# Kernel optimization log

Measured on AMD Instinct MI355X. Metric: run time of the kernel, lower is better.

The kernel has to match this reference:

```python
import jax, jax.numpy as jnp
import numpy as np

B, N, DIN, H, A = 4096, 32, 256, 128, 32  # batch, n_agents, din, hidden_dim, n_actions
NEG = 9e15


def _linear_params(key, fan_in, fan_out):
    kw, kb = jax.random.split(key)
    bound = 1.0 / np.sqrt(fan_in)
    w = jax.random.uniform(kw, (fan_in, fan_out), jnp.float32, -bound, bound)
    b = jax.random.uniform(kb, (fan_out,), jnp.float32, -bound, bound)
    return w, b


def setup_inputs() -> dict:
    key = jax.random.key(0)
    ks = jax.random.split(key, 12)
    x = jax.random.normal(ks[0], (B, N, DIN), jnp.float32)
    mask = jax.random.randint(ks[1], (B, N, N), 0, 2).astype(jnp.float32)
    enc_w, enc_b = _linear_params(ks[2], DIN, H)
    a1_vw, a1_vb = _linear_params(ks[3], H, H)
    a1_kw, a1_kb = _linear_params(ks[4], H, H)
    a1_qw, a1_qb = _linear_params(ks[5], H, H)
    a1_ow, a1_ob = _linear_params(ks[6], H, H)
    a2_vw, a2_vb = _linear_params(ks[7], H, H)
    a2_kw, a2_kb = _linear_params(ks[8], H, H)
    a2_qw, a2_qb = _linear_params(ks[9], H, H)
    a2_ow, a2_ob = _linear_params(ks[10], H, H)
    q_w, q_b = _linear_params(ks[11], H, A)
    return dict(x=x, mask=mask, enc_w=enc_w, enc_b=enc_b,
                a1_vw=a1_vw, a1_vb=a1_vb, a1_kw=a1_kw, a1_kb=a1_kb,
                a1_qw=a1_qw, a1_qb=a1_qb, a1_ow=a1_ow, a1_ob=a1_ob,
                a2_vw=a2_vw, a2_vb=a2_vb, a2_kw=a2_kw, a2_kb=a2_kb,
                a2_qw=a2_qw, a2_qb=a2_qb, a2_ow=a2_ow, a2_ob=a2_ob,
                q_w=q_w, q_b=q_b)


def _att_block(h, mask, vw, vb, kw, kb, qw, qb, ow, ob):
    # h: [B, N, H]; mask: [B, N, N]
    v = jax.nn.relu(jnp.einsum('bnd,dh->bnh', h, vw) + vb)
    q = jax.nn.relu(jnp.einsum('bnd,dh->bnh', h, qw) + qb)
    k = jax.nn.relu(jnp.einsum('bnd,dh->bnh', h, kw) + kb)
    scores = jnp.einsum('bih,bjh->bij', q, k)               # [B, N, N]
    logits = scores * mask - NEG * (1.0 - mask)
    att = jax.nn.softmax(logits, axis=2)
    out = jnp.einsum('bij,bjh->bih', att, v)
    return jax.nn.relu(jnp.einsum('bnh,ho->bno', out, ow) + ob)


def reference(x, mask, enc_w, enc_b,
              a1_vw, a1_vb, a1_kw, a1_kb, a1_qw, a1_qb, a1_ow, a1_ob,
              a2_vw, a2_vb, a2_kw, a2_kb, a2_qw, a2_qb, a2_ow, a2_ob,
              q_w, q_b):
    h1 = jax.nn.relu(jnp.einsum('bnd,dh->bnh', x, enc_w) + enc_b)
    h2 = _att_block(h1, mask, a1_vw, a1_vb, a1_kw, a1_kb, a1_qw, a1_qb, a1_ow, a1_ob)
    h3 = _att_block(h2, mask, a2_vw, a2_vb, a2_kw, a2_kb, a2_qw, a2_qb, a2_ow, a2_ob)
    q = jnp.einsum('bnh,ha->bna', h3, q_w) + q_b            # [B, N, A]
    return q
```

## Files before the change

kernel.cpp:

```cpp
#include <hip/hip_runtime.h>
#include <hip/hip_bf16.h>

typedef __attribute__((ext_vector_type(8))) short bf16x8;
typedef __attribute__((ext_vector_type(4))) short bf16x4;
typedef __attribute__((ext_vector_type(4))) float f32x4;

#define DEVI static __device__ __forceinline__

constexpr int NAG = 32, DIN = 256, HDIM = 128, ADIM = 32;
constexpr int G = 2;

constexpr int WS_ENC = 0;
constexpr int WS_H   = 32768;
constexpr int WS_QW  = 32768 + 8 * 16384;
constexpr int WS_TOT = WS_QW + 4096;

constexpr int SH = 136;
constexpr int SV = 72;
constexpr int SA = 40;
constexpr int SX = 264;

constexpr int L_R0 = 0;
constexpr int L_R1 = 17408;
constexpr int L_R2 = 34816;
constexpr int L_RV = 52224;
constexpr int L_AT = 70656;
constexpr int L_TOT = 75776;

DEVI short f2bf(float f) {
  union { float f; unsigned u; } a; a.f = f;
  return (short)((a.u + 0x7fffu + ((a.u >> 16) & 1u)) >> 16);
}

__global__ void prep_weights(const float* __restrict__ enc_w,
                             const float* __restrict__ m0, const float* __restrict__ m1,
                             const float* __restrict__ m2, const float* __restrict__ m3,
                             const float* __restrict__ m4, const float* __restrict__ m5,
                             const float* __restrict__ m6, const float* __restrict__ m7,
                             const float* __restrict__ qw,
                             short* __restrict__ ws)
{
  const int blk = blockIdx.x, tid = threadIdx.x;
  const float* src; int base, NM, nsh, f4;
  if (blk < 32) { src = enc_w; base = WS_ENC; NM = 8; nsh = 7; f4 = blk * 256 + tid; }
  else if (blk < 160) {
    const int m = (blk - 32) >> 4;
    if      (m == 0) src = m0; else if (m == 1) src = m1;
    else if (m == 2) src = m2; else if (m == 3) src = m3;
    else if (m == 4) src = m4; else if (m == 5) src = m5;
    else if (m == 6) src = m6; else             src = m7;
    base = WS_H + (m << 14); NM = 8; nsh = 7; f4 = ((blk - 32) & 15) * 256 + tid;
  } else { src = qw; base = WS_QW; NM = 2; nsh = 5; f4 = (blk - 160) * 256 + tid; }
  const int s = f4 * 4;
  const int row = s >> nsh, col0 = s & ((1 << nsh) - 1);
  const float4 v = *(const float4*)(src + s);
  const int j = row & 7, ks = row >> 5, lhi = ((row >> 3) & 3) * 16;
  const float vv[4] = {v.x, v.y, v.z, v.w};
#pragma unroll
  for (int c = 0; c < 4; ++c) {
    const int col = col0 + c;
    const int mt = col >> 4, lane = lhi + (col & 15);
    ws[base + (((ks * NM + mt) * 64 + lane) << 3) + j] = f2bf(vv[c]);
  }
}

template<int KSTEPS, bool RELU>
DEVI void linearSw(const short* __restrict__ src, int sstride,
                   const short* __restrict__ wfrag, const float* __restrict__ bias,
                   short* __restrict__ dst,
                   int wave, int lr, int lq, int lane)
{
  const int mg = wave >> 1, ng = wave & 1;
  f32x4 acc[2][2];
#pragma unroll
  for (int a = 0; a < 2; ++a)
#pragma unroll
    for (int b = 0; b < 2; ++b) acc[a][b] = (f32x4){0.f, 0.f, 0.f, 0.f};

  const bf16x8* wp = (const bf16x8*)wfrag;
#pragma unroll
  for (int ks = 0; ks < KSTEPS; ++ks) {
    bf16x8 hb[2];
#pragma unroll
    for (int b = 0; b < 2; ++b)
      hb[b] = *(const bf16x8*)(src + ((ng * 2 + b) * 16 + lr) * sstride + ks * 32 + lq * 8);
    bf16x8 wa[2];
#pragma unroll
    for (int a = 0; a < 2; ++a)
      wa[a] = wp[(ks * 8 + mg * 2 + a) * 64 + lane];
#pragma unroll
    for (int a = 0; a < 2; ++a)
#pragma unroll
      for (int b = 0; b < 2; ++b)
        acc[a][b] = __builtin_amdgcn_mfma_f32_16x16x32_bf16(wa[a], hb[b], acc[a][b], 0, 0, 0);
  }
#pragma unroll
  for (int a = 0; a < 2; ++a) {
    const float4 bv = *(const float4*)(bias + (mg * 2 + a) * 16 + lq * 4);
    const float bb[4] = {bv.x, bv.y, bv.z, bv.w};
#pragma unroll
    for (int b = 0; b < 2; ++b) {
      bf16x4 s;
#pragma unroll
      for (int r = 0; r < 4; ++r) {
        float v = acc[a][b][r] + bb[r];
        if (RELU) v = fmaxf(v, 0.f);
        s[r] = f2bf(v);
      }
      *(bf16x4*)(dst + ((ng * 2 + b) * 16 + lr) * SH + (mg * 2 + a) * 16 + lq * 4) = s;
    }
  }
}

DEVI void qkv_pass(const short* __restrict__ h,
                   const short* __restrict__ wq, const short* __restrict__ wk,
                   const short* __restrict__ wv,
                   const float* __restrict__ bq, const float* __restrict__ bk,
                   const float* __restrict__ bv,
                   short* __restrict__ Q, short* __restrict__ K, short* __restrict__ V,
                   int wave, int lr, int lq, int lane)
{
  const int mg = wave >> 1, ng = wave & 1;
  f32x4 qa[2][2], ka[2][2], va[2][2];
#pragma unroll
  for (int a = 0; a < 2; ++a)
#pragma unroll
    for (int b = 0; b < 2; ++b) {
      qa[a][b] = (f32x4){0.f, 0.f, 0.f, 0.f};
      ka[a][b] = (f32x4){0.f, 0.f, 0.f, 0.f};
      va[a][b] = (f32x4){0.f, 0.f, 0.f, 0.f};
    }
  const bf16x8* wpq = (const bf16x8*)wq;
  const bf16x8* wpk = (const bf16x8*)wk;
  const bf16x8* wpv = (const bf16x8*)wv;
#pragma unroll
  for (int ks = 0; ks < 4; ++ks) {
    bf16x8 hf[2];
#pragma unroll
    for (int b = 0; b < 2; ++b)
      hf[b] = *(const bf16x8*)(h + ((ng * 2 + b) * 16 + lr) * SH + ks * 32 + lq * 8);
#pragma unroll
    for (int a = 0; a < 2; ++a) {
      const bf16x8 wqf = wpq[(ks * 8 + mg * 2 + a) * 64 + lane];
      const bf16x8 wkf = wpk[(ks * 8 + mg * 2 + a) * 64 + lane];
      const bf16x8 wvf = wpv[(ks * 8 + mg * 2 + a) * 64 + lane];
#pragma unroll
      for (int b = 0; b < 2; ++b) {
        qa[a][b] = __builtin_amdgcn_mfma_f32_16x16x32_bf16(wqf, hf[b], qa[a][b], 0, 0, 0);
        ka[a][b] = __builtin_amdgcn_mfma_f32_16x16x32_bf16(wkf, hf[b], ka[a][b], 0, 0, 0);
        va[b][a] = __builtin_amdgcn_mfma_f32_16x16x32_bf16(hf[b], wvf, va[b][a], 0, 0, 0);
      }
    }
  }
#pragma unroll
  for (int a = 0; a < 2; ++a) {
    const float4 bq4 = *(const float4*)(bq + (mg * 2 + a) * 16 + lq * 4);
    const float4 bk4 = *(const float4*)(bk + (mg * 2 + a) * 16 + lq * 4);
    const float qb4[4] = {bq4.x, bq4.y, bq4.z, bq4.w};
    const float kb4[4] = {bk4.x, bk4.y, bk4.z, bk4.w};
#pragma unroll
    for (int b = 0; b < 2; ++b) {
      bf16x4 sq, sk;
#pragma unroll
      for (int r = 0; r < 4; ++r) {
        sq[r] = f2bf(fmaxf(qa[a][b][r] + qb4[r], 0.f));
        sk[r] = f2bf(fmaxf(ka[a][b][r] + kb4[r], 0.f));
      }
      const int off = ((ng * 2 + b) * 16 + lr) * SH + (mg * 2 + a) * 16 + lq * 4;
      *(bf16x4*)(Q + off) = sq;
      *(bf16x4*)(K + off) = sk;
    }
  }
#pragma unroll
  for (int a = 0; a < 2; ++a) {
    const float bvv = bv[(mg * 2 + a) * 16 + lr];
#pragma unroll
    for (int b = 0; b < 2; ++b) {
      bf16x4 sv;
#pragma unroll
      for (int r = 0; r < 4; ++r)
        sv[r] = f2bf(fmaxf(va[b][a][r] + bvv, 0.f));
      *(bf16x4*)(V + ((mg * 2 + a) * 16 + lr) * SV + (ng * 2 + b) * 16 + lq * 4) = sv;
    }
  }
}

DEVI void scores_pass(const short* __restrict__ Q, const short* __restrict__ K,
                      short* __restrict__ AT, const float* __restrict__ mask, int b0,
                      int wave, int lr, int lq, int lane)
{
  const int g = wave >> 1, qt = wave & 1;
  f32x4 sc[2];
  sc[0] = (f32x4){0.f, 0.f, 0.f, 0.f};
  sc[1] = (f32x4){0.f, 0.f, 0.f, 0.f};
#pragma unroll
  for (int ks = 0; ks < 4; ++ks) {
    const bf16x8 qf = *(const bf16x8*)(Q + (g * 32 + qt * 16 + lr) * SH + ks * 32 + lq * 8);
#pragma unroll
    for (int kt = 0; kt < 2; ++kt) {
      const bf16x8 kf = *(const bf16x8*)(K + (g * 32 + kt * 16 + lr) * SH + ks * 32 + lq * 8);
      sc[kt] = __builtin_amdgcn_mfma_f32_16x16x32_bf16(kf, qf, sc[kt], 0, 0, 0);
    }
  }
  const float* mp = mask + (size_t)(b0 + g) * (NAG * NAG) + (qt * 16 + lr) * 32;
  float l[2][4];
  float M = -3.0e38f;
#pragma unroll
  for (int kt = 0; kt < 2; ++kt) {
    const float4 m4 = *(const float4*)(mp + kt * 16 + lq * 4);
    const float mm[4] = {m4.x, m4.y, m4.z, m4.w};
#pragma unroll
    for (int r = 0; r < 4; ++r) {
      const float v = sc[kt][r] * mm[r] - 9e15f * (1.f - mm[r]);
      l[kt][r] = v;
      M = fmaxf(M, v);
    }
  }
  M = fmaxf(M, __shfl_xor(M, 16));
  M = fmaxf(M, __shfl_xor(M, 32));
  float e[2][4], T = 0.f;
#pragma unroll
  for (int kt = 0; kt < 2; ++kt)
#pragma unroll
    for (int r = 0; r < 4; ++r) { e[kt][r] = __expf(l[kt][r] - M); T += e[kt][r]; }
  T += __shfl_xor(T, 16);
  T += __shfl_xor(T, 32);
  const float rT = __frcp_rn(T);
#pragma unroll
  for (int kt = 0; kt < 2; ++kt) {
    bf16x4 s;
#pragma unroll
    for (int r = 0; r < 4; ++r) s[r] = f2bf(e[kt][r] * rT);
    *(bf16x4*)(AT + (g * 32 + qt * 16 + lr) * SA + kt * 16 + lq * 4) = s;
  }
}

DEVI void pv_pass(const short* __restrict__ V, const short* __restrict__ AT,
                  short* __restrict__ AO, int wave, int lr, int lq, int lane)
{
  const int g = wave >> 2, qt = (wave >> 1) & 1, fh = wave & 1;
  const bf16x8 atf = *(const bf16x8*)(AT + (g * 32 + qt * 16 + lr) * SA + lq * 8);
  f32x4 pacc[4];
#pragma unroll
  for (int f = 0; f < 4; ++f) {
    const int ft = fh * 4 + f;
    const bf16x8 vf = *(const bf16x8*)(V + (ft * 16 + lr) * SV + g * 32 + lq * 8);
    pacc[f] = __builtin_amdgcn_mfma_f32_16x16x32_bf16(
        vf, atf, (f32x4){0.f, 0.f, 0.f, 0.f}, 0, 0, 0);
  }
#pragma unroll
  for (int f = 0; f < 4; ++f) {
    const int ft = fh * 4 + f;
    bf16x4 s;
#pragma unroll
    for (int r = 0; r < 4; ++r) s[r] = f2bf(pacc[f][r]);
    *(bf16x4*)(AO + (g * 32 + qt * 16 + lr) * SH + ft * 16 + lq * 4) = s;
  }
}

DEVI void att_block(short* Rh, short* Rq, short* RK, short* RV_, short* ATb,
                    const short* wv, const short* wk, const short* wq, const short* wo,
                    const float* bv, const float* bk, const float* bq, const float* bo,
                    const float* __restrict__ mask, int b0,
                    int wave, int lr, int lq, int lane)
{
  qkv_pass(Rh, wq, wk, wv, bq, bk, bv, Rq, RK, RV_, wave, lr, lq, lane);
  __syncthreads();
  if (wave < 4) scores_pass(Rq, RK, ATb, mask, b0, wave, lr, lq, lane);
  __syncthreads();
  pv_pass(RV_, ATb, Rh, wave, lr, lq, lane);
  __syncthreads();
  linearSw<4, true>(Rh, SH, wo, bo, Rq, wave, lr, lq, lane);
  __syncthreads();
}

__global__ __launch_bounds__(512, 4)
void dgn_main(const float* __restrict__ x, const float* __restrict__ mask,
              const float* __restrict__ enc_b,
              const float* __restrict__ b1v, const float* __restrict__ b1k,
              const float* __restrict__ b1q, const float* __restrict__ b1o,
              const float* __restrict__ b2v, const float* __restrict__ b2k,
              const float* __restrict__ b2q, const float* __restrict__ b2o,
              const float* __restrict__ qb,
              const short* __restrict__ wf,
              float* __restrict__ out)
{
  __shared__ __align__(16) char smem[L_TOT];
  short* R0 = (short*)(smem + L_R0);
  short* R1 = (short*)(smem + L_R1);
  short* R2 = (short*)(smem + L_R2);
  short* RV_ = (short*)(smem + L_RV);
  short* ATb = (short*)(smem + L_AT);
  short* XB = (short*)(smem + L_R1);

  const int tid = threadIdx.x;
  const int wave = tid >> 6, lane = tid & 63;
  const int lr = lane & 15, lq = lane >> 4;
  const int b0 = blockIdx.x * G;

  {
    const float4* xsrc = (const float4*)(x + (size_t)b0 * NAG * DIN);
#pragma unroll
    for (int it = 0; it < 8; ++it) {
      const int q4 = tid + it * 512;
      const float4 v = xsrc[q4];
      bf16x4 s;
      s[0] = f2bf(v.x); s[1] = f2bf(v.y); s[2] = f2bf(v.z); s[3] = f2bf(v.w);
      *(bf16x4*)(XB + (q4 >> 6) * SX + (q4 & 63) * 4) = s;
    }
  }
  __syncthreads();

  linearSw<8, true>(XB, SX, wf + WS_ENC, enc_b, R0, wave, lr, lq, lane);
  __syncthreads();

  att_block(R0, R1, R2, RV_, ATb,
            wf + WS_H + 0 * 16384, wf + WS_H + 1 * 16384,
            wf + WS_H + 2 * 16384, wf + WS_H + 3 * 16384,
            b1v, b1k, b1q, b1o, mask, b0, wave, lr, lq, lane);

  att_block(R1, R0, R2, RV_, ATb,
            wf + WS_H + 4 * 16384, wf + WS_H + 5 * 16384,
            wf + WS_H + 6 * 16384, wf + WS_H + 7 * 16384,
            b2v, b2k, b2q, b2o, mask, b0, wave, lr, lq, lane);

  if (wave < 4) {
    f32x4 ha[2];
    ha[0] = (f32x4){0.f, 0.f, 0.f, 0.f};
    ha[1] = (f32x4){0.f, 0.f, 0.f, 0.f};
    const bf16x8* wp = (const bf16x8*)(wf + WS_QW);
#pragma unroll
    for (int ks = 0; ks < 4; ++ks) {
      const bf16x8 hf = *(const bf16x8*)(R0 + (wave * 16 + lr) * SH + ks * 32 + lq * 8);
#pragma unroll
      for (int a = 0; a < 2; ++a)
        ha[a] = __builtin_amdgcn_mfma_f32_16x16x32_bf16(wp[(ks * 2 + a) * 64 + lane], hf, ha[a], 0, 0, 0);
    }
    const int row = wave * 16 + lr;
    float* op = out + (((size_t)(b0 + (row >> 5)) * NAG) + (row & 31)) * ADIM;
#pragma unroll
    for (int a = 0; a < 2; ++a) {
      const float4 bv4 = *(const float4*)(qb + a * 16 + lq * 4);
      float4 o;
      o.x = ha[a][0] + bv4.x; o.y = ha[a][1] + bv4.y;
      o.z = ha[a][2] + bv4.z; o.w = ha[a][3] + bv4.w;
      *(float4*)(op + a * 16 + lq * 4) = o;
    }
  }
}

extern "C" void kernel_launch(void* const* d_in, const int* in_sizes, int n_in,
                              void* d_out, int out_size, void* d_ws, size_t ws_size,
                              hipStream_t stream)
{
  const float* x     = (const float*)d_in[0];
  const float* mask  = (const float*)d_in[1];
  const float* enc_w = (const float*)d_in[2];
  const float* enc_b = (const float*)d_in[3];
  const float* a1_vw = (const float*)d_in[4];
  const float* a1_vb = (const float*)d_in[5];
  const float* a1_kw = (const float*)d_in[6];
  const float* a1_kb = (const float*)d_in[7];
  const float* a1_qw = (const float*)d_in[8];
  const float* a1_qb = (const float*)d_in[9];
  const float* a1_ow = (const float*)d_in[10];
  const float* a1_ob = (const float*)d_in[11];
  const float* a2_vw = (const float*)d_in[12];
  const float* a2_vb = (const float*)d_in[13];
  const float* a2_kw = (const float*)d_in[14];
  const float* a2_kb = (const float*)d_in[15];
  const float* a2_qw = (const float*)d_in[16];
  const float* a2_qb = (const float*)d_in[17];
  const float* a2_ow = (const float*)d_in[18];
  const float* a2_ob = (const float*)d_in[19];
  const float* q_w   = (const float*)d_in[20];
  const float* q_b   = (const float*)d_in[21];
  short* ws = (short*)d_ws;

  prep_weights<<<164, 256, 0, stream>>>(
      enc_w, a1_vw, a1_kw, a1_qw, a1_ow, a2_vw, a2_kw, a2_qw, a2_ow, q_w, ws);

  dgn_main<<<4096 / G, 512, 0, stream>>>(
      x, mask, enc_b,
      a1_vb, a1_kb, a1_qb, a1_ob,
      a2_vb, a2_kb, a2_qb, a2_ob,
      q_b, ws, (float*)d_out);
}
```

Baseline: 313.2 us.

## Process one batch element per 256-thread block with compact shared-memory layout

Each block now handles a single batch element with 4 waves instead of two elements with 8 waves. Shared-memory buffers are reorganised and aliased (Q/K/V, attention weights and outputs reuse regions), cutting LDS from about 74KB to about 36KB per block. The aim is more resident blocks per CU for better latency hiding. In exchange there are twice as many blocks, weight fragments are reloaded per block, and the softmax stage runs on only 2 of 4 waves.

```diff
diff --git a/kernel.cpp b/kernel.cpp
--- a/kernel.cpp
+++ b/kernel.cpp
@@ -8,7 +8,6 @@
 #define DEVI static __device__ __forceinline__
 
 constexpr int NAG = 32, DIN = 256, HDIM = 128, ADIM = 32;
-constexpr int G = 2;
 
 constexpr int WS_ENC = 0;
 constexpr int WS_H   = 32768;
@@ -16,16 +15,15 @@
 constexpr int WS_TOT = WS_QW + 4096;
 
 constexpr int SH = 136;
-constexpr int SV = 72;
+constexpr int SV = 40;
 constexpr int SA = 40;
 constexpr int SX = 264;
 
-constexpr int L_R0 = 0;
-constexpr int L_R1 = 17408;
-constexpr int L_R2 = 34816;
-constexpr int L_RV = 52224;
-constexpr int L_AT = 70656;
-constexpr int L_TOT = 75776;
+constexpr int L_P0 = 0;
+constexpr int L_P1 = 8704;
+constexpr int L_P2 = 17408;
+constexpr int L_PV = 26112;
+constexpr int L_TOT = 36352;
 
 DEVI short f2bf(float f) {
   union { float f; unsigned u; } a; a.f = f;
@@ -65,12 +63,11 @@
 }
 
 template<int KSTEPS, bool RELU>
-DEVI void linearSw(const short* __restrict__ src, int sstride,
-                   const short* __restrict__ wfrag, const float* __restrict__ bias,
-                   short* __restrict__ dst,
-                   int wave, int lr, int lq, int lane)
-{
-  const int mg = wave >> 1, ng = wave & 1;
+DEVI void linearSw4(const short* __restrict__ src, int sstride,
+                    const short* __restrict__ wfrag, const float* __restrict__ bias,
+                    short* __restrict__ dst,
+                    int mg, int lr, int lq, int lane)
+{
   f32x4 acc[2][2];
 #pragma unroll
   for (int a = 0; a < 2; ++a)
@@ -83,16 +80,14 @@
     bf16x8 hb[2];
 #pragma unroll
     for (int b = 0; b < 2; ++b)
-      hb[b] = *(const bf16x8*)(src + ((ng * 2 + b) * 16 + lr) * sstride + ks * 32 + lq * 8);
-    bf16x8 wa[2];
-#pragma unroll
-    for (int a = 0; a < 2; ++a)
-      wa[a] = wp[(ks * 8 + mg * 2 + a) * 64 + lane];
-#pragma unroll
-    for (int a = 0; a < 2; ++a)
+      hb[b] = *(const bf16x8*)(src + (b * 16 + lr) * sstride + ks * 32 + lq * 8);
+#pragma unroll
+    for (int a = 0; a < 2; ++a) {
+      const bf16x8 wa = wp[(ks * 8 + mg * 2 + a) * 64 + lane];
 #pragma unroll
       for (int b = 0; b < 2; ++b)
-        acc[a][b] = __builtin_amdgcn_mfma_f32_16x16x32_bf16(wa[a], hb[b], acc[a][b], 0, 0, 0);
+        acc[a][b] = __builtin_amdgcn_mfma_f32_16x16x32_bf16(wa, hb[b], acc[a][b], 0, 0, 0);
+    }
   }
 #pragma unroll
   for (int a = 0; a < 2; ++a) {
@@ -107,20 +102,19 @@
         if (RELU) v = fmaxf(v, 0.f);
         s[r] = f2bf(v);
       }
-      *(bf16x4*)(dst + ((ng * 2 + b) * 16 + lr) * SH + (mg * 2 + a) * 16 + lq * 4) = s;
-    }
-  }
-}
-
-DEVI void qkv_pass(const short* __restrict__ h,
-                   const short* __restrict__ wq, const short* __restrict__ wk,
-                   const short* __restrict__ wv,
-                   const float* __restrict__ bq, const float* __restrict__ bk,
-                   const float* __restrict__ bv,
-                   short* __restrict__ Q, short* __restrict__ K, short* __restrict__ V,
-                   int wave, int lr, int lq, int lane)
-{
-  const int mg = wave >> 1, ng = wave & 1;
+      *(bf16x4*)(dst + (b * 16 + lr) * SH + (mg * 2 + a) * 16 + lq * 4) = s;
+    }
+  }
+}
+
+DEVI void qkv_pass4(const short* __restrict__ h,
+                    const short* __restrict__ wq, const short* __restrict__ wk,
+                    const short* __restrict__ wv,
+                    const float* __restrict__ bq, const float* __restrict__ bk,
+                    const float* __restrict__ bv,
+                    short* __restrict__ Q, short* __restrict__ K, short* __restrict__ V,
+                    int mg, int lr, int lq, int lane)
+{
   f32x4 qa[2][2], ka[2][2], va[2][2];
 #pragma unroll
   for (int a = 0; a < 2; ++a)
@@ -138,7 +132,7 @@
     bf16x8 hf[2];
 #pragma unroll
     for (int b = 0; b < 2; ++b)
-      hf[b] = *(const bf16x8*)(h + ((ng * 2 + b) * 16 + lr) * SH + ks * 32 + lq * 8);
+      hf[b] = *(const bf16x8*)(h + (b * 16 + lr) * SH + ks * 32 + lq * 8);
 #pragma unroll
     for (int a = 0; a < 2; ++a) {
       const bf16x8 wqf = wpq[(ks * 8 + mg * 2 + a) * 64 + lane];
@@ -166,7 +160,7 @@
         sq[r] = f2bf(fmaxf(qa[a][b][r] + qb4[r], 0.f));
         sk[r] = f2bf(fmaxf(ka[a][b][r] + kb4[r], 0.f));
       }
-      const int off = ((ng * 2 + b) * 16 + lr) * SH + (mg * 2 + a) * 16 + lq * 4;
+      const int off = (b * 16 + lr) * SH + (mg * 2 + a) * 16 + lq * 4;
       *(bf16x4*)(Q + off) = sq;
       *(bf16x4*)(K + off) = sk;
     }
@@ -180,29 +174,28 @@
 #pragma unroll
       for (int r = 0; r < 4; ++r)
         sv[r] = f2bf(fmaxf(va[b][a][r] + bvv, 0.f));
-      *(bf16x4*)(V + ((mg * 2 + a) * 16 + lr) * SV + (ng * 2 + b) * 16 + lq * 4) = sv;
-    }
-  }
-}
-
-DEVI void scores_pass(const short* __restrict__ Q, const short* __restrict__ K,
-                      short* __restrict__ AT, const float* __restrict__ mask, int b0,
-                      int wave, int lr, int lq, int lane)
-{
-  const int g = wave >> 1, qt = wave & 1;
+      *(bf16x4*)(V + ((mg * 2 + a) * 16 + lr) * SV + b * 16 + lq * 4) = sv;
+    }
+  }
+}
+
+DEVI void scores_pass4(const short* __restrict__ Q, const short* __restrict__ K,
+                       short* __restrict__ AT, const float* __restrict__ mask,
+                       int b0, int qt, int lr, int lq)
+{
   f32x4 sc[2];
   sc[0] = (f32x4){0.f, 0.f, 0.f, 0.f};
   sc[1] = (f32x4){0.f, 0.f, 0.f, 0.f};
 #pragma unroll
   for (int ks = 0; ks < 4; ++ks) {
-    const bf16x8 qf = *(const bf16x8*)(Q + (g * 32 + qt * 16 + lr) * SH + ks * 32 + lq * 8);
+    const bf16x8 qf = *(const bf16x8*)(Q + (qt * 16 + lr) * SH + ks * 32 + lq * 8);
 #pragma unroll
     for (int kt = 0; kt < 2; ++kt) {
-      const bf16x8 kf = *(const bf16x8*)(K + (g * 32 + kt * 16 + lr) * SH + ks * 32 + lq * 8);
+      const bf16x8 kf = *(const bf16x8*)(K + (kt * 16 + lr) * SH + ks * 32 + lq * 8);
       sc[kt] = __builtin_amdgcn_mfma_f32_16x16x32_bf16(kf, qf, sc[kt], 0, 0, 0);
     }
   }
-  const float* mp = mask + (size_t)(b0 + g) * (NAG * NAG) + (qt * 16 + lr) * 32;
+  const float* mp = mask + (size_t)b0 * (NAG * NAG) + (qt * 16 + lr) * 32;
   float l[2][4];
   float M = -3.0e38f;
 #pragma unroll
@@ -231,50 +224,51 @@
     bf16x4 s;
 #pragma unroll
     for (int r = 0; r < 4; ++r) s[r] = f2bf(e[kt][r] * rT);
-    *(bf16x4*)(AT + (g * 32 + qt * 16 + lr) * SA + kt * 16 + lq * 4) = s;
-  }
-}
-
-DEVI void pv_pass(const short* __restrict__ V, const short* __restrict__ AT,
-                  short* __restrict__ AO, int wave, int lr, int lq, int lane)
-{
-  const int g = wave >> 2, qt = (wave >> 1) & 1, fh = wave & 1;
-  const bf16x8 atf = *(const bf16x8*)(AT + (g * 32 + qt * 16 + lr) * SA + lq * 8);
-  f32x4 pacc[4];
-#pragma unroll
-  for (int f = 0; f < 4; ++f) {
-    const int ft = fh * 4 + f;
-    const bf16x8 vf = *(const bf16x8*)(V + (ft * 16 + lr) * SV + g * 32 + lq * 8);
-    pacc[f] = __builtin_amdgcn_mfma_f32_16x16x32_bf16(
-        vf, atf, (f32x4){0.f, 0.f, 0.f, 0.f}, 0, 0, 0);
-  }
-#pragma unroll
-  for (int f = 0; f < 4; ++f) {
-    const int ft = fh * 4 + f;
-    bf16x4 s;
-#pragma unroll
-    for (int r = 0; r < 4; ++r) s[r] = f2bf(pacc[f][r]);
-    *(bf16x4*)(AO + (g * 32 + qt * 16 + lr) * SH + ft * 16 + lq * 4) = s;
-  }
-}
-
-DEVI void att_block(short* Rh, short* Rq, short* RK, short* RV_, short* ATb,
-                    const short* wv, const short* wk, const short* wq, const short* wo,
-                    const float* bv, const float* bk, const float* bq, const float* bo,
-                    const float* __restrict__ mask, int b0,
-                    int wave, int lr, int lq, int lane)
-{
-  qkv_pass(Rh, wq, wk, wv, bq, bk, bv, Rq, RK, RV_, wave, lr, lq, lane);
-  __syncthreads();
-  if (wave < 4) scores_pass(Rq, RK, ATb, mask, b0, wave, lr, lq, lane);
-  __syncthreads();
-  pv_pass(RV_, ATb, Rh, wave, lr, lq, lane);
-  __syncthreads();
-  linearSw<4, true>(Rh, SH, wo, bo, Rq, wave, lr, lq, lane);
-  __syncthreads();
-}
-
-__global__ __launch_bounds__(512, 4)
+    *(bf16x4*)(AT + (qt * 16 + lr) * SA + kt * 16 + lq * 4) = s;
+  }
+}
+
+DEVI void pv_pass4(const short* __restrict__ V, const short* __restrict__ AT,
+                   short* __restrict__ AO, int wave, int lr, int lq)
+{
+  bf16x8 atf[2];
+#pragma unroll
+  for (int qt = 0; qt < 2; ++qt)
+    atf[qt] = *(const bf16x8*)(AT + (qt * 16 + lr) * SA + lq * 8);
+#pragma unroll
+  for (int fi = 0; fi < 2; ++fi) {
+    const int f2 = wave * 2 + fi;
+    const bf16x8 vf = *(const bf16x8*)(V + (f2 * 16 + lr) * SV + lq * 8);
+#pragma unroll
+    for (int qt = 0; qt < 2; ++qt) {
+      const f32x4 p = __builtin_amdgcn_mfma_f32_16x16x32_bf16(
+          vf, atf[qt], (f32x4){0.f, 0.f, 0.f, 0.f}, 0, 0, 0);
+      bf16x4 s;
+#pragma unroll
+      for (int r = 0; r < 4; ++r) s[r] = f2bf(p[r]);
+      *(bf16x4*)(AO + (qt * 16 + lr) * SH + f2 * 16 + lq * 4) = s;
+    }
+  }
+}
+
+DEVI void att_block4(const short* Rh, short* RQ, short* RK, short* RV,
+                     short* RAT, short* RAO, short* Rout,
+                     const short* wv, const short* wk, const short* wq, const short* wo,
+                     const float* bv, const float* bk, const float* bq, const float* bo,
+                     const float* __restrict__ mask, int b0,
+                     int wave, int lr, int lq, int lane)
+{
+  qkv_pass4(Rh, wq, wk, wv, bq, bk, bv, RQ, RK, RV, wave, lr, lq, lane);
+  __syncthreads();
+  if (wave < 2) scores_pass4(RQ, RK, RAT, mask, b0, wave, lr, lq);
+  __syncthreads();
+  pv_pass4(RV, RAT, RAO, wave, lr, lq);
+  __syncthreads();
+  linearSw4<4, true>(RAO, SH, wo, bo, Rout, wave, lr, lq, lane);
+  __syncthreads();
+}
+
+__global__ __launch_bounds__(256, 4)
 void dgn_main(const float* __restrict__ x, const float* __restrict__ mask,
               const float* __restrict__ enc_b,
               const float* __restrict__ b1v, const float* __restrict__ b1k,
@@ -286,23 +280,22 @@
               float* __restrict__ out)
 {
   __shared__ __align__(16) char smem[L_TOT];
-  short* R0 = (short*)(smem + L_R0);
-  short* R1 = (short*)(smem + L_R1);
-  short* R2 = (short*)(smem + L_R2);
-  short* RV_ = (short*)(smem + L_RV);
-  short* ATb = (short*)(smem + L_AT);
-  short* XB = (short*)(smem + L_R1);
+  short* P0 = (short*)(smem + L_P0);
+  short* P1 = (short*)(smem + L_P1);
+  short* P2 = (short*)(smem + L_P2);
+  short* PV = (short*)(smem + L_PV);
+  short* XB = (short*)(smem + L_P1);
 
   const int tid = threadIdx.x;
   const int wave = tid >> 6, lane = tid & 63;
   const int lr = lane & 15, lq = lane >> 4;
-  const int b0 = blockIdx.x * G;
+  const int b0 = blockIdx.x;
 
   {
     const float4* xsrc = (const float4*)(x + (size_t)b0 * NAG * DIN);
 #pragma unroll
     for (int it = 0; it < 8; ++it) {
-      const int q4 = tid + it * 512;
+      const int q4 = tid + it * 256;
       const float4 v = xsrc[q4];
       bf16x4 s;
       s[0] = f2bf(v.x); s[1] = f2bf(v.y); s[2] = f2bf(v.z); s[3] = f2bf(v.w);
@@ -311,33 +304,32 @@
   }
   __syncthreads();
 
-  linearSw<8, true>(XB, SX, wf + WS_ENC, enc_b, R0, wave, lr, lq, lane);
-  __syncthreads();
-
-  att_block(R0, R1, R2, RV_, ATb,
-            wf + WS_H + 0 * 16384, wf + WS_H + 1 * 16384,
-            wf + WS_H + 2 * 16384, wf + WS_H + 3 * 16384,
-            b1v, b1k, b1q, b1o, mask, b0, wave, lr, lq, lane);
-
-  att_block(R1, R0, R2, RV_, ATb,
-            wf + WS_H + 4 * 16384, wf + WS_H + 5 * 16384,
-            wf + WS_H + 6 * 16384, wf + WS_H + 7 * 16384,
-            b2v, b2k, b2q, b2o, mask, b0, wave, lr, lq, lane);
-
-  if (wave < 4) {
+  linearSw4<8, true>(XB, SX, wf + WS_ENC, enc_b, P0, wave, lr, lq, lane);
+  __syncthreads();
+
+  att_block4(P0, P1, P2, PV, P0, P1, P2,
+             wf + WS_H + 0 * 16384, wf + WS_H + 1 * 16384,
+             wf + WS_H + 2 * 16384, wf + WS_H + 3 * 16384,
+             b1v, b1k, b1q, b1o, mask, b0, wave, lr, lq, lane);
+
+  att_block4(P2, P0, P1, PV, P2, P0, P1,
+             wf + WS_H + 4 * 16384, wf + WS_H + 5 * 16384,
+             wf + WS_H + 6 * 16384, wf + WS_H + 7 * 16384,
+             b2v, b2k, b2q, b2o, mask, b0, wave, lr, lq, lane);
+
+  if (wave < 2) {
     f32x4 ha[2];
     ha[0] = (f32x4){0.f, 0.f, 0.f, 0.f};
     ha[1] = (f32x4){0.f, 0.f, 0.f, 0.f};
     const bf16x8* wp = (const bf16x8*)(wf + WS_QW);
 #pragma unroll
     for (int ks = 0; ks < 4; ++ks) {
-      const bf16x8 hf = *(const bf16x8*)(R0 + (wave * 16 + lr) * SH + ks * 32 + lq * 8);
+      const bf16x8 hf = *(const bf16x8*)(P1 + (wave * 16 + lr) * SH + ks * 32 + lq * 8);
 #pragma unroll
       for (int a = 0; a < 2; ++a)
         ha[a] = __builtin_amdgcn_mfma_f32_16x16x32_bf16(wp[(ks * 2 + a) * 64 + lane], hf, ha[a], 0, 0, 0);
     }
-    const int row = wave * 16 + lr;
-    float* op = out + (((size_t)(b0 + (row >> 5)) * NAG) + (row & 31)) * ADIM;
+    float* op = out + ((size_t)b0 * NAG + wave * 16 + lr) * ADIM;
 #pragma unroll
     for (int a = 0; a < 2; ++a) {
       const float4 bv4 = *(const float4*)(qb + a * 16 + lq * 4);
@@ -380,7 +372,7 @@
   prep_weights<<<164, 256, 0, stream>>>(
       enc_w, a1_vw, a1_kw, a1_qw, a1_ow, a2_vw, a2_kw, a2_qw, a2_ow, q_w, ws);
 
-  dgn_main<<<4096 / G, 512, 0, stream>>>(
+  dgn_main<<<4096, 256, 0, stream>>>(
       x, mask, enc_b,
       a1_vb, a1_kb, a1_qb, a1_ob,
       a2_vb, a2_kb, a2_qb, a2_ob,
```

Measured after the change: 290.2 us. 1.08x faster.
